# Kernel tuning notes

Hardware: AMD Instinct MI355X
Metric: run time of the kernel (lower is better)

The kernel has to match this reference:

```python
import jax, jax.numpy as jnp
import numpy as np

POOL = 7        # adaptive max pool output size
STRIDE = 16.0   # feature stride of VGG16 conv5


def _bin_masks(lo, hi, size, nbins=POOL):
    """Boolean masks [R, nbins, size]: pixel p belongs to adaptive-pool bin i
    of the region [lo, hi). PyTorch AdaptiveMaxPool2d bin boundaries:
    start = floor(i*L/n), end = ceil((i+1)*L/n), L = hi - lo."""
    L = hi - lo                                   # [R]
    i = jnp.arange(nbins, dtype=jnp.int32)
    starts = lo[:, None] + (i[None, :] * L[:, None]) // nbins          # [R, nbins]
    ends = lo[:, None] + ((i[None, :] + 1) * L[:, None] + nbins - 1) // nbins
    pos = jnp.arange(size, dtype=jnp.int32)
    return (pos[None, None, :] >= starts[..., None]) & (pos[None, None, :] < ends[..., None])


def roi_pool(x, rois):
    """x: [1,C,H,W]; rois: [R,4] = (y1,x1,y2,x2) in image pixels.
    Returns [R, C, POOL, POOL], matching the per-ROI slice + AdaptiveMaxPool2d loop."""
    xf = x[0]                                     # [C,H,W]
    C, H, W = xf.shape
    h0 = (rois[:, 0] / STRIDE).astype(jnp.int32)
    h1 = (rois[:, 2] / STRIDE).astype(jnp.int32) + 1
    w0 = (rois[:, 1] / STRIDE).astype(jnp.int32)
    w1 = (rois[:, 3] / STRIDE).astype(jnp.int32) + 1
    mH = _bin_masks(h0, h1, H)                    # [R,7,H]
    mW = _bin_masks(w0, w1, W)                    # [R,7,W]
    NEG = jnp.finfo(xf.dtype).min
    # reduce over W per w-bin (small fixed loop over 7 bins keeps memory bounded)
    colmax = jnp.stack(
        [jnp.where(mW[:, wb][:, None, None, :], xf[None], NEG).max(-1) for wb in range(POOL)],
        axis=-1)                                  # [R,C,H,7]
    # reduce over H per h-bin
    pooled = jnp.stack(
        [jnp.where(mH[:, hb][:, None, :, None], colmax, NEG).max(2) for hb in range(POOL)],
        axis=2)                                   # [R,C,7,7]
    return pooled


def setup_inputs() -> dict:
    key = jax.random.key(0)
    ks = jax.random.split(key, 10)
    H_img, W_img = 16 * 37, 16 * 50
    x = jax.random.normal(ks[0], (1, 512, 37, 50), dtype=jnp.float32)
    R = 128
    y1 = jax.random.uniform(ks[1], (R,), minval=0.0, maxval=H_img - 32.0)
    x1 = jax.random.uniform(ks[2], (R,), minval=0.0, maxval=W_img - 32.0)
    hh = jax.random.uniform(ks[3], (R,), minval=16.0, maxval=256.0)
    ww = jax.random.uniform(ks[4], (R,), minval=16.0, maxval=256.0)
    y2 = jnp.minimum(y1 + hh, H_img - 1.0)
    x2 = jnp.minimum(x1 + ww, W_img - 1.0)
    rois = jnp.stack([y1, x1, y2, x2], axis=1).astype(jnp.float32)
    D_in, D_h = 512 * POOL * POOL, 4096
    n_class = 21
    W1 = jax.random.normal(ks[5], (D_in, D_h), dtype=jnp.float32) * 0.01
    b1 = jnp.zeros((D_h,), jnp.float32)
    W2 = jax.random.normal(ks[6], (D_h, D_h), dtype=jnp.float32) * 0.01
    b2 = jnp.zeros((D_h,), jnp.float32)
    Wloc = jax.random.normal(ks[7], (D_h, n_class * 4), dtype=jnp.float32) * 0.001
    bloc = jnp.zeros((n_class * 4,), jnp.float32)
    Wscore = jax.random.normal(ks[8], (D_h, n_class), dtype=jnp.float32) * 0.01
    bscore = jnp.zeros((n_class,), jnp.float32)
    return {"x": x, "rois": rois, "W1": W1, "b1": b1, "W2": W2, "b2": b2,
            "Wloc": Wloc, "bloc": bloc, "Wscore": Wscore, "bscore": bscore}


def reference(x, rois, W1, b1, W2, b2, Wloc, bloc, Wscore, bscore):
    pooled = roi_pool(x, rois)                    # [R,512,7,7]
    flat = pooled.reshape(pooled.shape[0], -1)    # [R,25088]
    fc6 = jax.nn.relu(flat @ W1 + b1)
    fc7 = jax.nn.relu(fc6 @ W2 + b2)
    roi_locs = fc7 @ Wloc + bloc                  # [R, n_class*4]
    roi_scores = fc7 @ Wscore + bscore            # [R, n_class]
    return roi_locs, roi_scores
```

## Files before the change

kernel.cpp:

```cpp
#include <hip/hip_runtime.h>
#include <hip/hip_bf16.h>


typedef __attribute__((ext_vector_type(8))) short bf16x8;
typedef __attribute__((ext_vector_type(4))) float f32x4;
typedef __attribute__((ext_vector_type(4))) short s16x4;

typedef const __attribute__((address_space(1))) void gvoid;
typedef __attribute__((address_space(3))) void lvoid;
#define GLD_LDS16(gp, lp) __builtin_amdgcn_global_load_lds((gvoid*)(gp), (lvoid*)(lp), 16, 0, 0)

#define WAITV8() { asm volatile("s_waitcnt vmcnt(8)" ::: "memory"); __builtin_amdgcn_sched_barrier(0); }
#define WAITV0() { asm volatile("s_waitcnt vmcnt(0)" ::: "memory"); __builtin_amdgcn_sched_barrier(0); }
#define BAR() { __builtin_amdgcn_sched_barrier(0); __builtin_amdgcn_s_barrier(); __builtin_amdgcn_sched_barrier(0); }

static __device__ __forceinline__ short f2bf(float f) {
  unsigned u = __builtin_bit_cast(unsigned, f);
  u += 0x7fffu + ((u >> 16) & 1u);
  return (short)(u >> 16);
}

__global__ __launch_bounds__(256) void roipool_kernel(
    const float* __restrict__ x, const float* __restrict__ rois,
    __hip_bfloat16* __restrict__ A) {
  const int cg = blockIdx.x;
  const int r  = blockIdx.y;
  const float y1 = rois[r*4+0], x1 = rois[r*4+1], y2 = rois[r*4+2], x2 = rois[r*4+3];
  const int h0 = (int)(y1 * 0.0625f);
  const int h1 = (int)(y2 * 0.0625f) + 1;
  const int w0 = (int)(x1 * 0.0625f);
  const int w1 = (int)(x2 * 0.0625f) + 1;
  const int Hh = h1 - h0, Ww = w1 - w0;
  const int n = Hh * Ww;
  __shared__ float tile[16][292];
  const int cl = threadIdx.x >> 4, i = threadIdx.x & 15;
  const int c = cg*16 + cl;
  const float* xc = x + c*1850 + h0*50 + w0;
  for (int p = i; p < n; p += 16) {
    int rr = p / Ww, cc = p - rr*Ww;
    tile[cl][p] = xc[rr*50 + cc];
  }
  __syncthreads();
  __hip_bfloat16* Arow = A + (size_t)r*25088 + c*49;
  for (int b = i; b < 49; b += 16) {
    int hb = b / 7, wb = b - hb*7;
    int rs = (hb*Hh)/7,  re = ((hb+1)*Hh + 6)/7;
    int cs = (wb*Ww)/7,  ce = ((wb+1)*Ww + 6)/7;
    float m = -3.402823466e38f;
    for (int rr2 = rs; rr2 < re; ++rr2)
      for (int cc2 = cs; cc2 < ce; ++cc2)
        m = fmaxf(m, tile[cl][rr2*Ww + cc2]);
    Arow[b] = __float2bfloat16(m);
  }
}

__global__ __launch_bounds__(256) void gemm_kernel(
    const __hip_bfloat16* __restrict__ A,
    const float* __restrict__ B,
    float* __restrict__ part,
    int K, int KC) {
  __shared__ short lA[2][8192];
  __shared__ float lB[2][4096];
  const int t = threadIdx.x;
  const int w = t >> 6, l = t & 63;
  const int bid = blockIdx.x;
  const int s  = bid & 7;
  const int nb = bid >> 3;
  const int kc0 = s * KC;
  const int Arow_bytes = K * 2;

  int aoff[4], boff[4];
#pragma unroll
  for (int p = 0; p < 4; ++p) {
    int o = (p*256 + t) * 16;
    int oa = o ^ (((o >> 7) & 7) << 4);
    aoff[p] = (oa >> 7) * Arow_bytes + (oa & 127);
    int ob = o ^ (((o >> 11) & 1) << 6);
    boff[p] = (ob >> 8) * 16384 + (ob & 255);
  }
  const int r15 = l & 15, kh = l >> 4;
  const int xa = (r15 & 7) << 4;
  const int aoj0 = r15*128 + ((kh*16) ^ xa);
  const int aoj1 = r15*128 + (((64) + kh*16) ^ xa);
  const int bo0  = ((kh*8)*256 + (w*16 + r15)*4) ^ ((kh & 1) << 6);

  const char* Ak = (const char*)A + kc0*2;
  const char* Bk = (const char*)B + (size_t)kc0*16384 + nb*256;

  f32x4 acc[8] = {};
  const int steps = KC >> 6;
  int cur = 0;

#pragma unroll
  for (int p = 0; p < 4; ++p) {
    GLD_LDS16(Ak + aoff[p], (char*)lA[0] + (p*256 + w*64)*16);
    GLD_LDS16(Bk + boff[p], (char*)lB[0] + (p*256 + w*64)*16);
  }
  Ak += 128; Bk += 64 * 16384;

  for (int st = 0; st < steps; ++st) {
    if (st + 1 < steps) {
      char* dA = (char*)lA[cur ^ 1];
      char* dB = (char*)lB[cur ^ 1];
#pragma unroll
      for (int p = 0; p < 4; ++p) {
        GLD_LDS16(Ak + aoff[p], dA + (p*256 + w*64)*16);
        GLD_LDS16(Bk + boff[p], dB + (p*256 + w*64)*16);
      }
      Ak += 128; Bk += 64 * 16384;
      WAITV8();
    } else {
      WAITV0();
    }
    BAR();
    const char* lAb = (const char*)lA[cur];
    const char* lBb = (const char*)lB[cur];
#pragma unroll
    for (int j = 0; j < 2; ++j) {
      const int ao = j ? aoj1 : aoj0;
      const int bo = (j ? 8192 : 0) + bo0;
      float bf[8];
#pragma unroll
      for (int i2 = 0; i2 < 8; ++i2)
        bf[i2] = *(const float*)(lBb + bo + i2*256);
      bf16x8 bfrag;
#pragma unroll
      for (int i2 = 0; i2 < 8; ++i2) bfrag[i2] = f2bf(bf[i2]);
#pragma unroll
      for (int mf = 0; mf < 8; ++mf) {
        bf16x8 afrag = *(const bf16x8*)(lAb + mf*2048 + ao);
        acc[mf] = __builtin_amdgcn_mfma_f32_16x16x32_bf16(afrag, bfrag, acc[mf], 0, 0, 0);
      }
    }
    BAR();
    cur ^= 1;
  }
  const int n = nb*64 + w*16 + r15;
  float* prow = part + (size_t)s*524288 + n;
#pragma unroll
  for (int mf = 0; mf < 8; ++mf) {
    int m0 = mf*16 + kh*4;
#pragma unroll
    for (int q = 0; q < 4; ++q)
      prow[(m0 + q)*4096] = acc[mf][q];
  }
}

template <int OUTF32>
__global__ __launch_bounds__(256) void reduce_kernel(
    const float* __restrict__ part, const float* __restrict__ bias,
    void* __restrict__ outp) {
  const int idx = (blockIdx.x*256 + threadIdx.x) * 4;
  f32x4 sum = {};
#pragma unroll
  for (int s2 = 0; s2 < 8; ++s2)
    sum += *(const f32x4*)(part + (size_t)s2*524288 + idx);
  sum += *(const f32x4*)(bias + (idx & 4095));
  if (OUTF32) {
    f32x4 o;
#pragma unroll
    for (int q = 0; q < 4; ++q) o[q] = fmaxf(sum[q], 0.f);
    *(f32x4*)((float*)outp + idx) = o;
  } else {
    s16x4 o;
#pragma unroll
    for (int q = 0; q < 4; ++q) o[q] = f2bf(fmaxf(sum[q], 0.f));
    *(s16x4*)((short*)outp + idx) = o;
  }
}

__global__ __launch_bounds__(512) void final_kernel(
    const float* __restrict__ fc7,
    const float* __restrict__ Wloc, const float* __restrict__ bloc,
    const float* __restrict__ Wscore, const float* __restrict__ bscore,
    float* __restrict__ out) {
  __shared__ float row[4096];
  __shared__ float psum[4][128];
  const int r = blockIdx.x, t = threadIdx.x;
  const float* src = fc7 + (size_t)r*4096;
  for (int i = t; i < 1024; i += 512)
    *(f32x4*)&row[i*4] = *(const f32x4*)&src[i*4];
  __syncthreads();
  const int c = t & 127, ks = t >> 7;
  float acc = 0.f;
  if (c < 105) {
    const float* W; int stride, cc;
    if (c < 84) { W = Wloc; stride = 84; cc = c; }
    else        { W = Wscore; stride = 21; cc = c - 84; }
    const int k0 = ks * 1024;
#pragma unroll 4
    for (int k = k0; k < k0 + 1024; ++k)
      acc = fmaf(row[k], W[(size_t)k*stride + cc], acc);
  }
  psum[ks][c] = acc;
  __syncthreads();
  if (ks == 0 && c < 105) {
    float v = psum[0][c] + psum[1][c] + psum[2][c] + psum[3][c];
    if (c < 84) out[(size_t)r*84 + c] = v + bloc[c];
    else        out[10752 + (size_t)r*21 + (c - 84)] = v + bscore[c - 84];
  }
}

extern "C" void kernel_launch(void* const* d_in, const int* in_sizes, int n_in,
                              void* d_out, int out_size, void* d_ws, size_t ws_size,
                              hipStream_t stream) {
  const float* x      = (const float*)d_in[0];
  const float* rois   = (const float*)d_in[1];
  const float* W1     = (const float*)d_in[2];
  const float* b1     = (const float*)d_in[3];
  const float* W2     = (const float*)d_in[4];
  const float* b2     = (const float*)d_in[5];
  const float* Wloc   = (const float*)d_in[6];
  const float* bloc   = (const float*)d_in[7];
  const float* Wscore = (const float*)d_in[8];
  const float* bscore = (const float*)d_in[9];
  float* out = (float*)d_out;

  char* ws = (char*)d_ws;
  __hip_bfloat16* Apool = (__hip_bfloat16*)(ws);
  short*          fc6   = (short*)(ws + 6422528);
  float*          fc7   = (float*)(ws + 7471104);
  float*          part  = (float*)(ws + 9568256);

  roipool_kernel<<<dim3(32, 128), 256, 0, stream>>>(x, rois, Apool);
  gemm_kernel<<<512, 256, 0, stream>>>(Apool, W1, part, 25088, 3136);
  reduce_kernel<0><<<512, 256, 0, stream>>>(part, b1, (void*)fc6);
  gemm_kernel<<<512, 256, 0, stream>>>((const __hip_bfloat16*)fc6, W2, part, 4096, 512);
  reduce_kernel<1><<<512, 256, 0, stream>>>(part, b2, (void*)fc7);
  final_kernel<<<128, 512, 0, stream>>>(fc7, Wloc, bloc, Wscore, bscore, out);
}
```

Before: 256.6 us.

## Fuse split-K reductions into GEMM tail and final kernel via atomic counters

```diff
diff --git a/kernel.cpp b/kernel.cpp
--- a/kernel.cpp
+++ b/kernel.cpp
@@ -22,7 +22,9 @@
 
 __global__ __launch_bounds__(256) void roipool_kernel(
     const float* __restrict__ x, const float* __restrict__ rois,
-    __hip_bfloat16* __restrict__ A) {
+    __hip_bfloat16* __restrict__ A, int* __restrict__ cnt) {
+  if (blockIdx.x == 0 && blockIdx.y == 0 && threadIdx.x < 64)
+    cnt[threadIdx.x * 16] = 0;
   const int cg = blockIdx.x;
   const int r  = blockIdx.y;
   const float y1 = rois[r*4+0], x1 = rois[r*4+1], y2 = rois[r*4+2], x2 = rois[r*4+3];
@@ -54,13 +56,18 @@
   }
 }
 
+template <int TAIL>
 __global__ __launch_bounds__(256) void gemm_kernel(
     const __hip_bfloat16* __restrict__ A,
     const float* __restrict__ B,
     float* __restrict__ part,
-    int K, int KC) {
+    int K, int KC,
+    const float* __restrict__ bias,
+    short* __restrict__ fcout,
+    int* __restrict__ cnt) {
   __shared__ short lA[2][8192];
   __shared__ float lB[2][4096];
+  __shared__ int s_old;
   const int t = threadIdx.x;
   const int w = t >> 6, l = t & 63;
   const int bid = blockIdx.x;
@@ -144,42 +151,52 @@
     for (int q = 0; q < 4; ++q)
       prow[(m0 + q)*4096] = acc[mf][q];
   }
-}
-
-template <int OUTF32>
-__global__ __launch_bounds__(256) void reduce_kernel(
-    const float* __restrict__ part, const float* __restrict__ bias,
-    void* __restrict__ outp) {
-  const int idx = (blockIdx.x*256 + threadIdx.x) * 4;
-  f32x4 sum = {};
-#pragma unroll
-  for (int s2 = 0; s2 < 8; ++s2)
-    sum += *(const f32x4*)(part + (size_t)s2*524288 + idx);
-  sum += *(const f32x4*)(bias + (idx & 4095));
-  if (OUTF32) {
-    f32x4 o;
-#pragma unroll
-    for (int q = 0; q < 4; ++q) o[q] = fmaxf(sum[q], 0.f);
-    *(f32x4*)((float*)outp + idx) = o;
-  } else {
-    s16x4 o;
-#pragma unroll
-    for (int q = 0; q < 4; ++q) o[q] = f2bf(fmaxf(sum[q], 0.f));
-    *(s16x4*)((short*)outp + idx) = o;
+
+  if (TAIL) {
+    if (t == 0)
+      s_old = __hip_atomic_fetch_add(&cnt[nb * 16], 1, __ATOMIC_ACQ_REL,
+                                     __HIP_MEMORY_SCOPE_AGENT);
+    __syncthreads();
+    if (s_old == 7) {
+      __builtin_amdgcn_fence(__ATOMIC_ACQUIRE, "agent");
+#pragma unroll
+      for (int it = 0; it < 8; ++it) {
+        const int e = it*256 + t;
+        const int m = e >> 4;
+        const int col = nb*64 + (e & 15)*4;
+        f32x4 sum = {};
+#pragma unroll
+        for (int s2 = 0; s2 < 8; ++s2)
+          sum += *(const f32x4*)(part + (size_t)s2*524288 + m*4096 + col);
+        sum += *(const f32x4*)(bias + col);
+        s16x4 o;
+#pragma unroll
+        for (int q = 0; q < 4; ++q) o[q] = f2bf(fmaxf(sum[q], 0.f));
+        *(s16x4*)(fcout + (size_t)m*4096 + col) = o;
+      }
+    }
   }
 }
 
 __global__ __launch_bounds__(512) void final_kernel(
-    const float* __restrict__ fc7,
+    const float* __restrict__ part, const float* __restrict__ b2,
     const float* __restrict__ Wloc, const float* __restrict__ bloc,
     const float* __restrict__ Wscore, const float* __restrict__ bscore,
     float* __restrict__ out) {
   __shared__ float row[4096];
   __shared__ float psum[4][128];
   const int r = blockIdx.x, t = threadIdx.x;
-  const float* src = fc7 + (size_t)r*4096;
-  for (int i = t; i < 1024; i += 512)
-    *(f32x4*)&row[i*4] = *(const f32x4*)&src[i*4];
+  for (int ci = t; ci < 1024; ci += 512) {
+    f32x4 sum = {};
+#pragma unroll
+    for (int s2 = 0; s2 < 8; ++s2)
+      sum += *(const f32x4*)(part + (size_t)s2*524288 + r*4096 + ci*4);
+    sum += *(const f32x4*)(b2 + ci*4);
+    f32x4 o;
+#pragma unroll
+    for (int q = 0; q < 4; ++q) o[q] = fmaxf(sum[q], 0.f);
+    *(f32x4*)&row[ci*4] = o;
+  }
   __syncthreads();
   const int c = t & 127, ks = t >> 7;
   float acc = 0.f;
@@ -219,13 +236,13 @@
   char* ws = (char*)d_ws;
   __hip_bfloat16* Apool = (__hip_bfloat16*)(ws);
   short*          fc6   = (short*)(ws + 6422528);
-  float*          fc7   = (float*)(ws + 7471104);
   float*          part  = (float*)(ws + 9568256);
-
-  roipool_kernel<<<dim3(32, 128), 256, 0, stream>>>(x, rois, Apool);
-  gemm_kernel<<<512, 256, 0, stream>>>(Apool, W1, part, 25088, 3136);
-  reduce_kernel<0><<<512, 256, 0, stream>>>(part, b1, (void*)fc6);
-  gemm_kernel<<<512, 256, 0, stream>>>((const __hip_bfloat16*)fc6, W2, part, 4096, 512);
-  reduce_kernel<1><<<512, 256, 0, stream>>>(part, b2, (void*)fc7);
-  final_kernel<<<128, 512, 0, stream>>>(fc7, Wloc, bloc, Wscore, bscore, out);
-}
+  int*            cnt   = (int*)(ws + 26345472);
+
+  roipool_kernel<<<dim3(32, 128), 256, 0, stream>>>(x, rois, Apool, cnt);
+  gemm_kernel<1><<<512, 256, 0, stream>>>(Apool, W1, part, 25088, 3136,
+                                          b1, fc6, cnt);
+  gemm_kernel<0><<<512, 256, 0, stream>>>((const __hip_bfloat16*)fc6, W2, part,
+                                          4096, 512, nullptr, nullptr, nullptr);
+  final_kernel<<<128, 512, 0, stream>>>(part, b2, Wloc, bloc, Wscore, bscore, out);
+}
```

New measurement: 277.3 us. +8.1%, slower.
